# Performance work log

Measured on AMD Instinct MI355X. Metric: run time of the kernel, lower is better.

Reference implementation:

```python
import jax, jax.numpy as jnp
import numpy as np

NUM_HEADS = 8
NUM_LANDMARKS = 64


def setup_inputs() -> dict:
    key = jax.random.key(0)
    k1, k2, k3, k4, k5 = jax.random.split(key, 5)
    B, N, C = 4, 8192, 512
    x = jax.random.normal(k1, (B, N, C), dtype=jnp.float32)
    qkv_w = jax.random.normal(k2, (C, 3 * C), dtype=jnp.float32) * (C ** -0.5)
    qkv_b = jax.random.normal(k3, (3 * C,), dtype=jnp.float32) * 0.01
    proj_w = jax.random.normal(k4, (C, C), dtype=jnp.float32) * (C ** -0.5)
    proj_b = jax.random.normal(k5, (C,), dtype=jnp.float32) * 0.01
    return {"x": x, "qkv_w": qkv_w, "qkv_b": qkv_b, "proj_w": proj_w, "proj_b": proj_b}


def reference(x, qkv_w, qkv_b, proj_w, proj_b):
    B, N, C = x.shape
    H = NUM_HEADS
    D = C // H
    m = min(NUM_LANDMARKS, N)
    scale = D ** -0.5

    # qkv projection -> [3, B, H, N, D]
    qkv = (x @ qkv_w + qkv_b).reshape(B, N, 3, H, D).transpose(2, 0, 3, 1, 4)
    q, k, v = qkv[0], qkv[1], qkv[2]

    if m >= N:
        attn = jax.nn.softmax(jnp.einsum('bhnd,bhkd->bhnk', q, k) * scale, axis=-1)
        out = attn @ v  # [B,H,N,D]
    else:
        # landmark indices: linspace(0, N-1, m).long()
        idx = jnp.linspace(0, N - 1, m).astype(jnp.int32)
        q_l = q[:, :, idx]  # [B,H,m,D]
        k_l = k[:, :, idx]  # [B,H,m,D]
        kernel_1 = jax.nn.softmax(jnp.einsum('bhnd,bhmd->bhnm', q, k_l) * scale, axis=-1)  # [B,H,N,m]
        kernel_2 = jax.nn.softmax(jnp.einsum('bhmd,bhkd->bhmk', q_l, k_l) * scale, axis=-1)  # [B,H,m,m]
        kernel_3 = jax.nn.softmax(jnp.einsum('bhmd,bhnd->bhmn', q_l, k) * scale, axis=-1)  # [B,H,m,N]
        k2_inv = jnp.linalg.pinv(kernel_2)  # [B,H,m,m]
        # fuse right-to-left to keep intermediates small: [B,H,m,D]
        out = kernel_1 @ (k2_inv @ (kernel_3 @ v))  # [B,H,N,D]

    out = out.transpose(0, 2, 1, 3).reshape(B, N, C)
    return out @ proj_w + proj_b
```

## Files before the change

### kernel.cpp

```cpp
#include <hip/hip_runtime.h>
#include <stdint.h>

using bf16x8 = __attribute__((ext_vector_type(8))) short;
using bf16x8_t = __attribute__((ext_vector_type(8))) __bf16;
using f32x4  = __attribute__((ext_vector_type(4))) float;
typedef unsigned short u16;
typedef unsigned int   u32;

#define DEVI static __device__ __forceinline__

typedef u32 __attribute__((address_space(1))) gu32;
typedef u32 __attribute__((address_space(3))) lu32;

DEVI u16 f2b(float f) {
  union { float f; u32 u; } v; v.f = f;
  u32 r = v.u + 0x7FFFu + ((v.u >> 16) & 1u);
  return (u16)(r >> 16);
}

DEVI f32x4 mfma16(bf16x8 a, bf16x8 b, f32x4 c) {
  return __builtin_amdgcn_mfma_f32_16x16x32_bf16(
      __builtin_bit_cast(bf16x8_t, a), __builtin_bit_cast(bf16x8_t, b), c, 0, 0, 0);
}

DEVI void gload16(const void* g, void* l) {
  __builtin_amdgcn_global_load_lds((const gu32*)(uintptr_t)g,
                                   (lu32*)(u32)(uintptr_t)l, 16, 0, 0);
}

DEVI int swz64(int row, int ch) { return row*64 + ((ch ^ (row & 7)) << 3); }

#define VMCNT0 asm volatile("s_waitcnt vmcnt(0)" ::: "memory")
#define LGKM0  asm volatile("s_waitcnt lgkmcnt(0)" ::: "memory")

__global__ void __launch_bounds__(256) k_cast_x(const float4* __restrict__ xin,
                                                uint4* __restrict__ xo, int n8) {
  int i = blockIdx.x * 256 + threadIdx.x;
  if (i >= n8) return;
  float4 a = xin[2*i], b = xin[2*i+1];
  uint4 o;
  o.x = ((u32)f2b(a.y) << 16) | f2b(a.x);
  o.y = ((u32)f2b(a.w) << 16) | f2b(a.z);
  o.z = ((u32)f2b(b.y) << 16) | f2b(b.x);
  o.w = ((u32)f2b(b.w) << 16) | f2b(b.z);
  xo[i] = o;
}

__global__ void __launch_bounds__(256) k_tcast(const float* __restrict__ w,
                                               u16* __restrict__ wt, int R, int Cc) {
  int o = blockIdx.x * 256 + threadIdx.x;
  if (o >= R * Cc) return;
  int c = o % R, j = o / R;
  wt[o] = f2b(w[(size_t)c * Cc + j]);
}

__global__ void __launch_bounds__(256) k_lmk(
    const float* __restrict__ x, const float* __restrict__ w,
    const float* __restrict__ bias, float* __restrict__ qlf,
    float* __restrict__ klf, u16* __restrict__ qlb, u16* __restrict__ klb) {
  __shared__ __align__(16) float xr[512];
  const int t = threadIdx.x;
  const int b = blockIdx.x >> 6, i = blockIdx.x & 63;
  const int idx = (i * 8191) / 63;
  const float4* xg = (const float4*)(x + ((size_t)b*8192 + idx)*512);
  if (t < 128) ((float4*)xr)[t] = xg[t];
  __syncthreads();

  const int o0 = t << 2;
  float4 acc = *(const float4*)(bias + o0);
  const float* wp = w + o0;
  #pragma unroll 8
  for (int c = 0; c < 512; ++c) {
    const float xv = xr[c];
    const float4 wv = *(const float4*)(wp + (size_t)c*1536);
    acc.x = fmaf(xv, wv.x, acc.x); acc.y = fmaf(xv, wv.y, acc.y);
    acc.z = fmaf(xv, wv.z, acc.z); acc.w = fmaf(xv, wv.w, acc.w);
  }

  const int h = (o0 >> 6) & 7, d = o0 & 63;
  const size_t ofs = ((size_t)(b*8 + h)*64 + i)*64 + d;
  ushort4 pk;
  pk.x = f2b(acc.x); pk.y = f2b(acc.y); pk.z = f2b(acc.z); pk.w = f2b(acc.w);
  if (o0 < 512) { *(float4*)(qlf + ofs) = acc; *(ushort4*)(qlb + ofs) = pk; }
  else          { *(float4*)(klf + ofs) = acc; *(ushort4*)(klb + ofs) = pk; }
}

template <int MODE>
__global__ void __launch_bounds__(256) k_gemm(
    const u16* __restrict__ A, const u16* __restrict__ Bt,
    const float* __restrict__ bias, int K, int ntn,
    u16* __restrict__ qdst, u16* __restrict__ kdst, u16* __restrict__ vtdst,
    float* __restrict__ fout, int Nout,
    const float* __restrict__ qlf, const float* __restrict__ klf,
    float* __restrict__ invg) {
  constexpr int SMEM_BYTES = (MODE == 0) ? 34064 : 32768;
  __shared__ __align__(16) char smem[SMEM_BYTES];
  const int t = threadIdx.x;
  const int cpx = gridDim.x >> 3;
  const int wgid = (blockIdx.x & 7) * cpx + (blockIdx.x >> 3);

  if (MODE == 0 && wgid < 32) {
    float* Am = (float*)smem;
    int* pivcol = (int*)(smem + 33792);
    int* piv_sp = (int*)(smem + 33792 + 256);
    float4* A4 = (float4*)Am;
    const int bh = wgid;
    const int i4 = t >> 2, jc = t & 3;

    const float4* kg = (const float4*)(klf + (size_t)bh*4096);
    for (int g = t; g < 1024; g += 256) {
      int j = g >> 4, d4 = g & 15;
      ((float4*)(Am + j*132 + 64))[d4] = kg[g];
    }
    __syncthreads();

    {
      float4 qreg[16];
      const float4* qg = (const float4*)(qlf + (size_t)bh*4096 + (size_t)i4*64);
      #pragma unroll
      for (int q4 = 0; q4 < 16; ++q4) qreg[q4] = qg[q4];
      #pragma unroll
      for (int jj = 0; jj < 16; ++jj) {
        int j = jc*16 + jj;
        const float4* kv4 = (const float4*)(Am + j*132 + 64);
        float acc = 0.f;
        #pragma unroll
        for (int q4 = 0; q4 < 16; ++q4) {
          float4 kv = kv4[q4];
          acc = fmaf(qreg[q4].x, kv.x, acc); acc = fmaf(qreg[q4].y, kv.y, acc);
          acc = fmaf(qreg[q4].z, kv.z, acc); acc = fmaf(qreg[q4].w, kv.w, acc);
        }
        Am[i4*132 + j] = acc * 0.125f;
      }
    }
    __syncthreads();

    {
      float z[16]; float m = -1e30f;
      #pragma unroll
      for (int jj = 0; jj < 16; ++jj) { z[jj] = Am[i4*132 + jc*16 + jj]; m = fmaxf(m, z[jj]); }
      m = fmaxf(m, __shfl_xor(m, 1)); m = fmaxf(m, __shfl_xor(m, 2));
      float s = 0.f;
      #pragma unroll
      for (int jj = 0; jj < 16; ++jj) { z[jj] = __expf(z[jj] - m); s += z[jj]; }
      s += __shfl_xor(s, 1); s += __shfl_xor(s, 2);
      float rinv = 1.f / s;
      #pragma unroll
      for (int jj = 0; jj < 16; ++jj) {
        int j = jc*16 + jj;
        Am[i4*132 + j] = z[jj] * rinv;
        Am[i4*132 + 64 + j] = (j == i4) ? 1.f : 0.f;
      }
    }
    __syncthreads();

    const int r = i4, q = jc;
    int used = 0;
    for (int c = 0; c < 64; ++c) {
      if (t < 64) {
        float val = used ? -1.f : fabsf(Am[t*132 + c]);
        int idx = t;
        #pragma unroll
        for (int mk = 1; mk < 64; mk <<= 1) {
          float ov = __shfl_xor(val, mk);
          int oi = __shfl_xor(idx, mk);
          int take = (ov > val) || (ov == val && oi < idx);
          val = take ? ov : val;
          idx = take ? oi : idx;
        }
        if (t == idx) { used = 1; pivcol[t] = c; }
        if (t == 0) *piv_sp = idx;
      }
      __syncthreads();
      const int p = *piv_sp;
      if (r != p) {
        const float coef = -Am[r*132 + c] / Am[p*132 + c];
        const float4* Ap = A4 + p*33 + q*8;
        float4* Ar = A4 + r*33 + q*8;
        #pragma unroll
        for (int i = 0; i < 8; ++i) {
          float4 a = Ar[i], pv = Ap[i];
          a.x = fmaf(coef, pv.x, a.x); a.y = fmaf(coef, pv.y, a.y);
          a.z = fmaf(coef, pv.z, a.z); a.w = fmaf(coef, pv.w, a.w);
          Ar[i] = a;
        }
      }
      __syncthreads();
    }

    {
      const int cr = pivcol[r];
      const float rd = 1.f / Am[r*132 + cr];
      float4* og = (float4*)(invg + (size_t)bh*4096 + (size_t)cr*64) + q*4;
      #pragma unroll
      for (int i = 0; i < 4; ++i) {
        float4 v = A4[r*33 + 16 + q*4 + i];
        v.x *= rd; v.y *= rd; v.z *= rd; v.w *= rd;
        og[i] = v;
      }
    }
    return;
  }

  u16* As = (u16*)smem;
  u16* Bs = (u16*)(smem + 16384);
  const int wg2 = wgid - (MODE == 0 ? 32 : 0);
  const int tn = wg2 % ntn, tm = wg2 / ntn;
  const int m0 = tm << 7, n0 = tn << 7;
  const int w = t >> 6, l = t & 63;
  const int wr = (w >> 1) << 6, wc = (w & 1) << 6;
  const int lhi = l >> 4, llo = l & 15;

  f32x4 acc[4][4];
  #pragma unroll
  for (int i = 0; i < 4; ++i)
    #pragma unroll
    for (int j = 0; j < 4; ++j) acc[i][j] = f32x4{0.f,0.f,0.f,0.f};

  const int csw = (((t & 7) ^ ((t >> 3) & 7)) << 3);
  const u16* ga = A  + (size_t)(m0 + (t >> 3)) * K + csw;
  const u16* gb = Bt + (size_t)(n0 + (t >> 3)) * K + csw;
  u16* lA = As + (w << 9);
  u16* lB = Bs + (w << 9);

  for (int kt = 0; kt < K; kt += 64) {
    __syncthreads();
    #pragma unroll
    for (int i = 0; i < 4; ++i) {
      gload16(ga + (size_t)(i*32)*K + kt, lA + i*2048);
      gload16(gb + (size_t)(i*32)*K + kt, lB + i*2048);
    }
    VMCNT0;
    __syncthreads();
    #pragma unroll
    for (int kko = 0; kko < 64; kko += 32) {
      const int kc = kko >> 3;
      bf16x8 av[4], bv[4];
      #pragma unroll
      for (int mi = 0; mi < 4; ++mi)
        av[mi] = *(const bf16x8*)(As + swz64(wr + mi*16 + llo, kc + lhi));
      #pragma unroll
      for (int ni = 0; ni < 4; ++ni)
        bv[ni] = *(const bf16x8*)(Bs + swz64(wc + ni*16 + llo, kc + lhi));
      #pragma unroll
      for (int mi = 0; mi < 4; ++mi)
        #pragma unroll
        for (int ni = 0; ni < 4; ++ni)
          acc[mi][ni] = mfma16(av[mi], bv[ni], acc[mi][ni]);
    }
  }

  #pragma unroll
  for (int ni = 0; ni < 4; ++ni) {
    const int gcol = n0 + wc + ni*16 + llo;
    const float bvv = bias[gcol];
    if (MODE == 0) {
      const int tt = gcol >> 9, h = (gcol >> 6) & 7, d = gcol & 63;
      #pragma unroll
      for (int mi = 0; mi < 4; ++mi) {
        const int grow = m0 + wr + mi*16 + (lhi << 2);
        const int b = grow >> 13, n = grow & 8191;
        const size_t bh = (size_t)(b*8 + h);
        if (tt == 2) {
          ushort4 pk;
          pk.x = f2b(acc[mi][ni][0] + bvv); pk.y = f2b(acc[mi][ni][1] + bvv);
          pk.z = f2b(acc[mi][ni][2] + bvv); pk.w = f2b(acc[mi][ni][3] + bvv);
          *(ushort4*)(vtdst + (bh*64 + d)*8192 + n) = pk;
        } else {
          u16* dst = (tt == 0 ? qdst : kdst) + (bh*8192 + n)*64 + d;
          #pragma unroll
          for (int r = 0; r < 4; ++r) dst[(size_t)r*64] = f2b(acc[mi][ni][r] + bvv);
        }
      }
    } else {
      #pragma unroll
      for (int mi = 0; mi < 4; ++mi) {
        const int grow = m0 + wr + mi*16 + (lhi << 2);
        #pragma unroll
        for (int r = 0; r < 4; ++r)
          fout[(size_t)(grow + r)*Nout + gcol] = acc[mi][ni][r] + bvv;
      }
    }
  }
}

__global__ void __launch_bounds__(256) k_flash3(
    const u16* __restrict__ qlb, const u16* __restrict__ kmat,
    const u16* __restrict__ vt, float* __restrict__ num_part,
    float* __restrict__ den_part) {
  __shared__ __align__(16) u16 QL[64*64];
  __shared__ __align__(16) u16 KT[4][64*64];
  __shared__ __align__(16) u16 VT[4][64*64];
  __shared__ __align__(16) u16 PL[4][64*64];
  const int t = threadIdx.x, w = t >> 6, l = t & 63;
  const int bh = blockIdx.x >> 3, split = blockIdx.x & 7;
  const int lhi = l >> 4, llo = l & 15;
  const int csw = ((l & 7) ^ (l >> 3)) << 3;

  #pragma unroll
  for (int i = 0; i < 2; ++i)
    gload16(qlb + (size_t)bh*4096 + (size_t)((i*256 + (t & ~7)) << 3)
                + (((t & 7) ^ ((t >> 3) & 7)) << 3),
            QL + i*2048 + (w << 9));
  VMCNT0;
  __syncthreads();

  f32x4 oacc[4][4];
  float dacc[4][4];
  #pragma unroll
  for (int a = 0; a < 4; ++a)
    #pragma unroll
    for (int bq = 0; bq < 4; ++bq) { oacc[a][bq] = f32x4{0.f,0.f,0.f,0.f}; dacc[a][bq] = 0.f; }

  const int nb = split << 10;
  u16* lk = KT[w]; u16* lv = VT[w]; u16* lp = PL[w];
  for (int j = 0; j < 4; ++j) {
    const int n0 = nb + ((w + 4*j) << 6);
    const u16* gk = kmat + ((size_t)bh*8192 + n0 + (l >> 3))*64 + csw;
    const u16* gv = vt   + ((size_t)bh*64 + (l >> 3))*8192 + n0 + csw;
    asm volatile("" ::: "memory");
    LGKM0;
    #pragma unroll
    for (int i = 0; i < 8; ++i) {
      gload16(gk + (size_t)(i*8)*64, lk + i*512);
      gload16(gv + (size_t)(i*8)*8192, lv + i*512);
    }
    VMCNT0;

    f32x4 s[4][4];
    #pragma unroll
    for (int qi = 0; qi < 4; ++qi)
      #pragma unroll
      for (int nj = 0; nj < 4; ++nj) s[qi][nj] = f32x4{0.f,0.f,0.f,0.f};
    #pragma unroll
    for (int kko = 0; kko < 64; kko += 32) {
      const int kc = kko >> 3;
      bf16x8 av[4], bv[4];
      #pragma unroll
      for (int qi = 0; qi < 4; ++qi)
        av[qi] = *(const bf16x8*)(QL + swz64(qi*16 + llo, kc + lhi));
      #pragma unroll
      for (int nj = 0; nj < 4; ++nj)
        bv[nj] = *(const bf16x8*)(lk + swz64(nj*16 + llo, kc + lhi));
      #pragma unroll
      for (int qi = 0; qi < 4; ++qi)
        #pragma unroll
        for (int nj = 0; nj < 4; ++nj)
          s[qi][nj] = mfma16(av[qi], bv[nj], s[qi][nj]);
    }
    #pragma unroll
    for (int qi = 0; qi < 4; ++qi) {
      float rs[4] = {0.f, 0.f, 0.f, 0.f};
      #pragma unroll
      for (int nj = 0; nj < 4; ++nj)
        #pragma unroll
        for (int r = 0; r < 4; ++r) {
          float p = __expf(s[qi][nj][r] * 0.125f);
          rs[r] += p;
          const int prow = qi*16 + lhi*4 + r, pcol = nj*16 + llo;
          lp[swz64(prow, pcol >> 3) + (pcol & 7)] = f2b(p);
        }
      #pragma unroll
      for (int r = 0; r < 4; ++r) {
        float v = rs[r];
        v += __shfl_xor(v, 1); v += __shfl_xor(v, 2);
        v += __shfl_xor(v, 4); v += __shfl_xor(v, 8);
        dacc[qi][r] += v;
      }
    }
    LGKM0;
    #pragma unroll
    for (int kko = 0; kko < 64; kko += 32) {
      const int kc = kko >> 3;
      bf16x8 pa[4], vb[4];
      #pragma unroll
      for (int qi = 0; qi < 4; ++qi)
        pa[qi] = *(const bf16x8*)(lp + swz64(qi*16 + llo, kc + lhi));
      #pragma unroll
      for (int dj = 0; dj < 4; ++dj)
        vb[dj] = *(const bf16x8*)(lv + swz64(dj*16 + llo, kc + lhi));
      #pragma unroll
      for (int qi = 0; qi < 4; ++qi)
        #pragma unroll
        for (int dj = 0; dj < 4; ++dj)
          oacc[qi][dj] = mfma16(pa[qi], vb[dj], oacc[qi][dj]);
    }
  }
  const int sw = (split << 2) + w;
  float* np = num_part + ((size_t)bh*32 + sw)*4096;
  #pragma unroll
  for (int qi = 0; qi < 4; ++qi)
    #pragma unroll
    for (int dj = 0; dj < 4; ++dj)
      #pragma unroll
      for (int r = 0; r < 4; ++r)
        np[(qi*16 + lhi*4 + r)*64 + dj*16 + llo] = oacc[qi][dj][r];
  if (llo == 0) {
    float* dp = den_part + ((size_t)bh*32 + sw)*64;
    #pragma unroll
    for (int qi = 0; qi < 4; ++qi)
      #pragma unroll
      for (int r = 0; r < 4; ++r)
        dp[qi*16 + lhi*4 + r] = dacc[qi][r];
  }
}

__global__ void __launch_bounds__(256) k_t1(
    const float* __restrict__ num_part, const float* __restrict__ den_part,
    float* __restrict__ t1g) {
  const int t = threadIdx.x;
  const int bh = blockIdx.x >> 2, ch = blockIdx.x & 3;
  const int f = ch*256 + t;
  const int m = f >> 4;
  const float4* ng = (const float4*)num_part + (size_t)bh*32*1024;
  float4 acc = {0.f, 0.f, 0.f, 0.f};
  float ds = 0.f;
  for (int s = 0; s < 32; ++s) {
    float4 v = ng[(size_t)s*1024 + f];
    acc.x += v.x; acc.y += v.y; acc.z += v.z; acc.w += v.w;
    ds += den_part[((size_t)bh*32 + s)*64 + m];
  }
  float r = 1.f / ds;
  acc.x *= r; acc.y *= r; acc.z *= r; acc.w *= r;
  ((float4*)t1g)[(size_t)bh*1024 + f] = acc;
}

__global__ void __launch_bounds__(256) k_t2(
    const float* __restrict__ invg, const float* __restrict__ t1g,
    float* __restrict__ t2t) {
  __shared__ __align__(16) float IV[64*68];
  __shared__ __align__(16) float T1[64*68];
  const int t = threadIdx.x;
  const int bh = blockIdx.x;
  const int i4 = t >> 2, jc = t & 3;
  float4* IV4 = (float4*)IV;
  float4* T14 = (float4*)T1;
  const float4* ig = (const float4*)(invg + (size_t)bh*4096);
  const float4* tg = (const float4*)(t1g + (size_t)bh*4096);
  #pragma unroll
  for (int k = 0; k < 4; ++k) {
    int g = k*256 + t, row = g >> 4, c4 = g & 15;
    IV4[row*17 + c4] = ig[g];
    T14[row*17 + c4] = tg[g];
  }
  __syncthreads();
  float acc[16];
  #pragma unroll
  for (int d = 0; d < 16; ++d) acc[d] = 0.f;
  for (int m = 0; m < 64; ++m) {
    float wv = IV[i4*68 + m];
    #pragma unroll
    for (int d4 = 0; d4 < 4; ++d4) {
      float4 tv = T14[m*17 + jc*4 + d4];
      acc[d4*4+0] = fmaf(wv, tv.x, acc[d4*4+0]);
      acc[d4*4+1] = fmaf(wv, tv.y, acc[d4*4+1]);
      acc[d4*4+2] = fmaf(wv, tv.z, acc[d4*4+2]);
      acc[d4*4+3] = fmaf(wv, tv.w, acc[d4*4+3]);
    }
  }
  #pragma unroll
  for (int dd = 0; dd < 16; ++dd) {
    int d = jc*16 + dd;
    t2t[((size_t)bh*64 + d)*64 + i4] = acc[dd];
  }
}

__global__ void __launch_bounds__(256) k_flash1(
    const u16* __restrict__ q, const u16* __restrict__ klb,
    const float* __restrict__ t2t, u16* __restrict__ oatt) {
  __shared__ __align__(16) u16 KL[64*64];
  __shared__ __align__(16) u16 T2[64*64];
  __shared__ __align__(16) u16 QT[4][64*64];
  __shared__ __align__(16) u16 PL[4][64*64];
  const int t = threadIdx.x, w = t >> 6, l = t & 63;
  const int bh = blockIdx.x >> 5, blk = blockIdx.x & 31;
  const int lhi = l >> 4, llo = l & 15;
  const int b = bh >> 3, h = bh & 7;
  const int csw = ((l & 7) ^ (l >> 3)) << 3;

  #pragma unroll
  for (int i = 0; i < 2; ++i)
    gload16(klb + (size_t)bh*4096 + (size_t)((i*256 + (t & ~7)) << 3)
                + (((t & 7) ^ ((t >> 3) & 7)) << 3),
            KL + i*2048 + (w << 9));
  for (int i = t; i < 4096; i += 256)
    T2[swz64(i >> 6, (i & 63) >> 3) + (i & 7)] = f2b(t2t[(size_t)bh*4096 + i]);
  VMCNT0;
  __syncthreads();

  const int n0 = (blk << 8) + (w << 6);
  const u16* gq = q + ((size_t)bh*8192 + n0 + (l >> 3))*64 + csw;
  u16* lq = QT[w]; u16* lp = PL[w];
  #pragma unroll
  for (int i = 0; i < 8; ++i) gload16(gq + (size_t)(i*8)*64, lq + i*512);
  VMCNT0;

  f32x4 s[4][4];
  #pragma unroll
  for (int qi = 0; qi < 4; ++qi)
    #pragma unroll
    for (int nj = 0; nj < 4; ++nj) s[qi][nj] = f32x4{0.f,0.f,0.f,0.f};
  #pragma unroll
  for (int kko = 0; kko < 64; kko += 32) {
    const int kc = kko >> 3;
    bf16x8 av[4], bv[4];
    #pragma unroll
    for (int qi = 0; qi < 4; ++qi)
      av[qi] = *(const bf16x8*)(lq + swz64(qi*16 + llo, kc + lhi));
    #pragma unroll
    for (int nj = 0; nj < 4; ++nj)
      bv[nj] = *(const bf16x8*)(KL + swz64(nj*16 + llo, kc + lhi));
    #pragma unroll
    for (int qi = 0; qi < 4; ++qi)
      #pragma unroll
      for (int nj = 0; nj < 4; ++nj)
        s[qi][nj] = mfma16(av[qi], bv[nj], s[qi][nj]);
  }
  float rcp_[4][4];
  #pragma unroll
  for (int qi = 0; qi < 4; ++qi) {
    float mx[4] = {-1e30f, -1e30f, -1e30f, -1e30f};
    #pragma unroll
    for (int nj = 0; nj < 4; ++nj)
      #pragma unroll
      for (int r = 0; r < 4; ++r) {
        float z = s[qi][nj][r] * 0.125f;
        s[qi][nj][r] = z;
        mx[r] = fmaxf(mx[r], z);
      }
    #pragma unroll
    for (int r = 0; r < 4; ++r) {
      float m = mx[r];
      m = fmaxf(m, __shfl_xor(m, 1)); m = fmaxf(m, __shfl_xor(m, 2));
      m = fmaxf(m, __shfl_xor(m, 4)); m = fmaxf(m, __shfl_xor(m, 8));
      mx[r] = m;
    }
    float rs[4] = {0.f, 0.f, 0.f, 0.f};
    #pragma unroll
    for (int nj = 0; nj < 4; ++nj)
      #pragma unroll
      for (int r = 0; r < 4; ++r) {
        float p = __expf(s[qi][nj][r] - mx[r]);
        rs[r] += p;
        const int prow = qi*16 + lhi*4 + r, pcol = nj*16 + llo;
        lp[swz64(prow, pcol >> 3) + (pcol & 7)] = f2b(p);
      }
    #pragma unroll
    for (int r = 0; r < 4; ++r) {
      float v = rs[r];
      v += __shfl_xor(v, 1); v += __shfl_xor(v, 2);
      v += __shfl_xor(v, 4); v += __shfl_xor(v, 8);
      rcp_[qi][r] = 1.0f / v;
    }
  }
  LGKM0;
  f32x4 o[4][4];
  #pragma unroll
  for (int qi = 0; qi < 4; ++qi)
    #pragma unroll
    for (int dj = 0; dj < 4; ++dj) o[qi][dj] = f32x4{0.f,0.f,0.f,0.f};
  #pragma unroll
  for (int kko = 0; kko < 64; kko += 32) {
    const int kc = kko >> 3;
    bf16x8 pa[4], tb[4];
    #pragma unroll
    for (int qi = 0; qi < 4; ++qi)
      pa[qi] = *(const bf16x8*)(lp + swz64(qi*16 + llo, kc + lhi));
    #pragma unroll
    for (int dj = 0; dj < 4; ++dj)
      tb[dj] = *(const bf16x8*)(T2 + swz64(dj*16 + llo, kc + lhi));
    #pragma unroll
    for (int qi = 0; qi < 4; ++qi)
      #pragma unroll
      for (int dj = 0; dj < 4; ++dj)
        o[qi][dj] = mfma16(pa[qi], tb[dj], o[qi][dj]);
  }
  #pragma unroll
  for (int qi = 0; qi < 4; ++qi)
    #pragma unroll
    for (int dj = 0; dj < 4; ++dj)
      #pragma unroll
      for (int r = 0; r < 4; ++r) {
        int n = n0 + qi*16 + lhi*4 + r;
        oatt[((size_t)b*8192 + n)*512 + h*64 + dj*16 + llo] = f2b(o[qi][dj][r] * rcp_[qi][r]);
      }
}

extern "C" void kernel_launch(void* const* d_in, const int* in_sizes, int n_in,
                              void* d_out, int out_size, void* d_ws, size_t ws_size,
                              hipStream_t stream) {
  const float* x      = (const float*)d_in[0];
  const float* qkv_w  = (const float*)d_in[1];
  const float* qkv_b  = (const float*)d_in[2];
  const float* proj_w = (const float*)d_in[3];
  const float* proj_b = (const float*)d_in[4];
  float* out = (float*)d_out;

  char* ws = (char*)d_ws;
  size_t off = 0;
  auto alloc = [&](size_t bytes) -> char* {
    char* p = ws + off;
    off += (bytes + 255) & ~(size_t)255;
    return p;
  };
  u16*   x_bf  = (u16*)  alloc(33554432);
  u16*   vt    = (u16*)  alloc(33554432);
  u16*   wqkvt = (u16*)  alloc(1572864);
  u16*   wprjt = (u16*)  alloc(524288);
  float* qlf   = (float*)alloc(524288);
  float* klf   = (float*)alloc(524288);
  u16*   qlb   = (u16*)  alloc(262144);
  u16*   klb   = (u16*)  alloc(262144);
  float* nump  = (float*)alloc(16777216);
  float* denp  = (float*)alloc(262144);
  float* t2t   = (float*)alloc(524288);
  float* t1g   = (float*)alloc(524288);
  float* invg  = (float*)alloc(524288);
  if (off > ws_size) return;

  u16* qm   = (u16*)d_out;
  u16* kmat = qm + 16777216;
  u16* oatt = x_bf;

  k_cast_x<<<8192, 256, 0, stream>>>((const float4*)x, (uint4*)x_bf, 2097152);
  k_tcast<<<3072, 256, 0, stream>>>(qkv_w, wqkvt, 512, 1536);
  k_tcast<<<1024, 256, 0, stream>>>(proj_w, wprjt, 512, 512);
  k_lmk<<<256, 256, 0, stream>>>(x, qkv_w, qkv_b, qlf, klf, qlb, klb);
  k_gemm<0><<<3104, 256, 0, stream>>>(x_bf, wqkvt, qkv_b, 512, 12, qm, kmat, vt,
                                      nullptr, 0, qlf, klf, invg);
  k_flash3<<<256, 256, 0, stream>>>(qlb, kmat, vt, nump, denp);
  k_t1<<<128, 256, 0, stream>>>(nump, denp, t1g);
  k_t2<<<32, 256, 0, stream>>>(invg, t1g, t2t);
  k_flash1<<<1024, 256, 0, stream>>>(qm, klb, t2t, oatt);
  k_gemm<1><<<1024, 256, 0, stream>>>(oatt, wprjt, proj_b, 512, 4, nullptr, nullptr,
                                      nullptr, out, 512, nullptr, nullptr, nullptr);
}
```

Baseline: 273.4 us.

## Fuse pivot search into elimination step to halve barriers in Gauss-Jordan loop

In the 64x64 pinv Gauss-Jordan block, pivot candidates for the next column are now written to a shared array during the current elimination update. Every wave then computes the argmax redundantly, so the separate pivot-search phase, its extra __syncthreads, and the shared pivot broadcast are gone. Each thread keeps its own pivot column in a register. This saves one barrier per column iteration, at the cost of redundant shuffles in every wave and more conditional logic in the inner update.

```diff
diff --git a/kernel.cpp b/kernel.cpp
--- a/kernel.cpp
+++ b/kernel.cpp
@@ -101,11 +101,11 @@
 
   if (MODE == 0 && wgid < 32) {
     float* Am = (float*)smem;
-    int* pivcol = (int*)(smem + 33792);
-    int* piv_sp = (int*)(smem + 33792 + 256);
+    float* cand = (float*)(smem + 33792);
     float4* A4 = (float4*)Am;
     const int bh = wgid;
     const int i4 = t >> 2, jc = t & 3;
+    const int l = t & 63;
 
     const float4* kg = (const float4*)(klf + (size_t)bh*4096);
     for (int g = t; g < 1024; g += 256) {
@@ -151,29 +151,30 @@
         Am[i4*132 + j] = z[jj] * rinv;
         Am[i4*132 + 64 + j] = (j == i4) ? 1.f : 0.f;
       }
+      if (jc == 0) cand[i4] = fabsf(z[0] * rinv);
     }
     __syncthreads();
 
     const int r = i4, q = jc;
-    int used = 0;
+    int rused = 0, mypivc = 0;
     for (int c = 0; c < 64; ++c) {
-      if (t < 64) {
-        float val = used ? -1.f : fabsf(Am[t*132 + c]);
-        int idx = t;
-        #pragma unroll
-        for (int mk = 1; mk < 64; mk <<= 1) {
-          float ov = __shfl_xor(val, mk);
-          int oi = __shfl_xor(idx, mk);
-          int take = (ov > val) || (ov == val && oi < idx);
-          val = take ? ov : val;
-          idx = take ? oi : idx;
-        }
-        if (t == idx) { used = 1; pivcol[t] = c; }
-        if (t == 0) *piv_sp = idx;
-      }
-      __syncthreads();
-      const int p = *piv_sp;
-      if (r != p) {
+      float val = cand[l];
+      int idx = l;
+      #pragma unroll
+      for (int mk = 1; mk < 64; mk <<= 1) {
+        float ov = __shfl_xor(val, mk);
+        int oi = __shfl_xor(idx, mk);
+        int take = (ov > val) || (ov == val && oi < idx);
+        val = take ? ov : val;
+        idx = take ? oi : idx;
+      }
+      const int p = idx;
+      const int nc = c + 1;
+      const int nslot = nc >> 2, nq = nc >> 5, nelem = nc & 3;
+      if (r == p) {
+        rused = 1; mypivc = c;
+        if (q == 0) cand[r] = -1e30f;
+      } else {
         const float coef = -Am[r*132 + c] / Am[p*132 + c];
         const float4* Ap = A4 + p*33 + q*8;
         float4* Ar = A4 + r*33 + q*8;
@@ -183,13 +184,18 @@
           a.x = fmaf(coef, pv.x, a.x); a.y = fmaf(coef, pv.y, a.y);
           a.z = fmaf(coef, pv.z, a.z); a.w = fmaf(coef, pv.w, a.w);
           Ar[i] = a;
+          if (c < 63 && q == nq && (q*8 + i) == nslot) {
+            const float nv = (nelem == 0) ? a.x : (nelem == 1) ? a.y
+                           : (nelem == 2) ? a.z : a.w;
+            cand[r] = rused ? -1e30f : fabsf(nv);
+          }
         }
       }
       __syncthreads();
     }
 
     {
-      const int cr = pivcol[r];
+      const int cr = mypivc;
       const float rd = 1.f / Am[r*132 + cr];
       float4* og = (float4*)(invg + (size_t)bh*4096 + (size_t)cr*64) + q*4;
       #pragma unroll
```

Measured after the change: 276.0 us. About the same (+0.9%).
